# Optimization experiments

Measured on AMD Instinct MI355X. Metric: run time of the kernel, lower is better.

## Reference

```python
import jax, jax.numpy as jnp
import numpy as np
from jax import lax

H_IMG = 128; W_IMG = 128; C_IN = 200; NCLS = 16
N0 = H_IMG * W_IMG; N1 = 4096; N2 = 1024
K = 16  # neighbors(15) + 1 self loop, as in __init__
EPS = 1e-5
SLOPE = 0.01  # LeakyReLU default


def _leaky(x):
    return jnp.where(x >= 0, x, SLOPE * x)


def _bn1d(H, g, b):
    # BatchNorm1d in training mode: batch stats over node dim
    mu = H.mean(0)
    var = H.var(0)
    return (H - mu) * lax.rsqrt(var + EPS) * g + b


def _bn2d(x, g, b):
    mu = x.mean((0, 2, 3), keepdims=True)
    var = x.var((0, 2, 3), keepdims=True)
    return (x - mu) * lax.rsqrt(var + EPS) * g[None, :, None, None] + b[None, :, None, None]


def _ssconv(x, g, b, pw, pb, dw, db):
    # BN -> 1x1 pointwise conv -> LeakyReLU -> depthwise 5x5 conv -> LeakyReLU
    y = _bn2d(x, g, b)
    y = lax.conv_general_dilated(y, pw, (1, 1), 'SAME', dimension_numbers=('NCHW', 'OIHW', 'NCHW')) + pb[None, :, None, None]
    y = _leaky(y)
    c = dw.shape[0]
    y = lax.conv_general_dilated(y, dw, (1, 1), 'SAME', feature_group_count=c, dimension_numbers=('NCHW', 'OIHW', 'NCHW')) + db[None, :, None, None]
    return _leaky(y)


def _gcn(H, g, b, wt, bt, wo, bo, nbr):
    # GCNLayer_PyG, neighbors>0 branch. nbr: [N, K] neighbor indices (col), center broadcast (row)
    Hn = _bn1d(H, g, b)
    th = Hn @ wt + bt            # [N, 128]
    out = Hn @ wo + bo           # [N, F]
    A = jax.nn.sigmoid(jnp.einsum('nkd,nd->nk', th[nbr], th))  # sigmoid(<theta[col], theta[row]>)
    A = jax.nn.softmax(A, axis=1)                              # softmax over K neighbors
    agg = jnp.einsum('nk,nkf->nf', A, out[nbr])                # weighted neighbor aggregate
    return _leaky(agg), A


def _forward(x, hg, hb, hpw, hpb, hdw, hdb,
             e0_g, e0_b, e0_wt, e0_bt, e0_wo, e0_bo,
             e1_g, e1_b, e1_wt, e1_bt, e1_wo, e1_bo,
             d0_g, d0_b, d0_wt, d0_bt, d0_wo, d0_bo,
             tg, tb, tpw, tpb, tdw, tdb, ws, wb,
             S0, S1, Shat0, Shat1, nbr_a, nbr_b):
    x4 = x.transpose(2, 0, 1)[None]                 # [1, C, H, W]
    h0 = _ssconv(x4, hg, hb, hpw, hpb, hdw, hdb)    # [1, 128, H, W]
    H = h0[0].transpose(1, 2, 0).reshape(N0, -1)    # [N0, 128]
    enc0 = H
    H = Shat0 @ H                                   # pool to [N1, 128]
    H, A0 = _gcn(H, e0_g, e0_b, e0_wt, e0_bt, e0_wo, e0_bo, nbr_a)  # [N1, 64]
    enc1 = H
    H = Shat1 @ H                                   # pool to [N2, 64]
    H, A1 = _gcn(H, e1_g, e1_b, e1_wt, e1_bt, e1_wo, e1_bo, nbr_b)  # [N2, 32]
    # decoder
    H = S1 @ H                                      # unpool [N1, 32]
    H = jnp.concatenate([H, enc1], axis=-1)         # [N1, 96]
    H, Ad = _gcn(H, d0_g, d0_b, d0_wt, d0_bt, d0_wo, d0_bo, nbr_a)  # [N1, 64]
    H = S0 @ H                                      # unpool [N0, 64]
    H = jnp.concatenate([H, enc0], axis=-1)         # [N0, 192]
    t = H.reshape(1, H_IMG, W_IMG, -1).transpose(0, 3, 1, 2)
    f = _ssconv(t, tg, tb, tpw, tpb, tdw, tdb)      # [1, 128, H, W]
    f = f[0].transpose(1, 2, 0).reshape(N0, -1)
    Y = jax.nn.softmax(f @ ws + wb, axis=-1)        # [N0, NCLS]
    return Y


def setup_inputs() -> dict:
    key = jax.random.key(0)
    cnt = [0]
    def rn(shape, s=0.05):
        cnt[0] += 1
        return jax.random.normal(jax.random.fold_in(key, cnt[0]), shape, jnp.float32) * s
    x = rn((H_IMG, W_IMG, C_IN), 1.0)
    # balanced hierarchical assignment matrices (one-hot rows)
    S0 = jnp.zeros((N0, N1), jnp.float32).at[jnp.arange(N0), jnp.arange(N0) // (N0 // N1)].set(1.0)
    S1 = jnp.zeros((N1, N2), jnp.float32).at[jnp.arange(N1), jnp.arange(N1) // (N1 // N2)].set(1.0)
    Shat0 = (S0 / S0.sum(0, keepdims=True)).T
    Shat1 = (S1 / S1.sum(0, keepdims=True)).T
    # positions: pixel grid pooled through Shat (as in HiGCN.__init__)
    gx, gy = jnp.meshgrid(jnp.arange(H_IMG), jnp.arange(W_IMG), indexing='ij')
    pos = jnp.stack([gx, gy], -1).reshape(N0, 2).astype(jnp.float32)
    posA = Shat0 @ pos
    posB = Shat1 @ posA
    def knn(p):
        d = ((p[:, None, :] - p[None, :, :]) ** 2).sum(-1)
        return jnp.argsort(d, axis=1)[:, :K].astype(jnp.int32)  # self included (loop=True)
    nbr_a = knn(posA)  # [N1, K], used by enc0 and dec0
    nbr_b = knn(posB)  # [N2, K], used by enc1
    inp = dict(x=x, S0=S0, S1=S1, Shat0=Shat0, Shat1=Shat1, nbr_a=nbr_a, nbr_b=nbr_b)
    inp.update(hg=jnp.ones(C_IN), hb=jnp.zeros(C_IN), hpw=rn((128, C_IN, 1, 1)),
               hpb=jnp.zeros(128), hdw=rn((128, 1, 5, 5)), hdb=jnp.zeros(128))
    for tag, ci, co in (('e0', 128, 64), ('e1', 64, 32), ('d0', 96, 64)):
        inp[tag + '_g'] = jnp.ones(ci); inp[tag + '_b'] = jnp.zeros(ci)
        inp[tag + '_wt'] = rn((ci, 128)); inp[tag + '_bt'] = jnp.zeros(128)
        inp[tag + '_wo'] = rn((ci, co)); inp[tag + '_bo'] = jnp.zeros(co)
    inp.update(tg=jnp.ones(192), tb=jnp.zeros(192), tpw=rn((128, 192, 1, 1)),
               tpb=jnp.zeros(128), tdw=rn((128, 1, 5, 5)), tdb=jnp.zeros(128))
    inp.update(ws=rn((128, NCLS)), wb=jnp.zeros(NCLS))
    return inp


def reference(x, hg, hb, hpw, hpb, hdw, hdb,
              e0_g, e0_b, e0_wt, e0_bt, e0_wo, e0_bo,
              e1_g, e1_b, e1_wt, e1_bt, e1_wo, e1_bo,
              d0_g, d0_b, d0_wt, d0_bt, d0_wo, d0_bo,
              tg, tb, tpw, tpb, tdw, tdb, ws, wb,
              S0, S1, Shat0, Shat1, nbr_a, nbr_b):
    return _forward(x, hg, hb, hpw, hpb, hdw, hdb,
                    e0_g, e0_b, e0_wt, e0_bt, e0_wo, e0_bo,
                    e1_g, e1_b, e1_wt, e1_bt, e1_wo, e1_bo,
                    d0_g, d0_b, d0_wt, d0_bt, d0_wo, d0_bo,
                    tg, tb, tpw, tpb, tdw, tdb, ws, wb,
                    S0, S1, Shat0, Shat1, nbr_a, nbr_b)
```

## Files before the change

kernel.cpp:

```cpp
#include <hip/hip_runtime.h>
#include <hip/hip_bf16.h>
#include <math.h>

using bf16 = __hip_bfloat16;

#define H_IMG 128
#define W_IMG 128
#define C_IN  200
#define NCLS  16
#define N0    16384
#define N1    4096
#define N2    1024
#define KNB   16
#define EPS   1e-5f
#define SLOPE 0.01f

__device__ __forceinline__ float ldf(const float* p, long i) { return p[i]; }
__device__ __forceinline__ float ldf(const bf16* p, long i) { return __bfloat162float(p[i]); }
__device__ __forceinline__ float ldw(const void* p, long i, int fl) {
    return fl ? ((const float*)p)[i] : __bfloat162float(((const bf16*)p)[i]);
}
__device__ __forceinline__ float leaky(float v) { return v >= 0.f ? v : SLOPE * v; }

__device__ __forceinline__ float4 ld4(const float* p, long i) {
    return *reinterpret_cast<const float4*>(p + i);
}
__device__ __forceinline__ float4 ld4(const bf16* p, long i) {
    const ushort4 u = *reinterpret_cast<const ushort4*>(reinterpret_cast<const unsigned short*>(p) + i);
    float4 r;
    r.x = __uint_as_float((unsigned)u.x << 16);
    r.y = __uint_as_float((unsigned)u.y << 16);
    r.z = __uint_as_float((unsigned)u.z << 16);
    r.w = __uint_as_float((unsigned)u.w << 16);
    return r;
}

__device__ __forceinline__ int block_detect(const unsigned short* __restrict__ x) {
    __shared__ int cnt_s;
    if (threadIdx.x == 0) cnt_s = 0;
    __syncthreads();
    int cnt = 0;
    for (int i = threadIdx.x; i < 4096; i += blockDim.x) {
        unsigned short e = (unsigned short)((x[i] >> 7) & 0xFF);
        if (e >= 0xC0) cnt++;
    }
#pragma unroll
    for (int off = 32; off > 0; off >>= 1) cnt += __shfl_xor(cnt, off, 64);
    if ((threadIdx.x & 63) == 0) atomicAdd(&cnt_s, cnt);
    __syncthreads();
    return cnt_s > 32 ? 1 : 0;
}

__global__ __launch_bounds__(256) void bnx_kernel(const void* __restrict__ X, float2* __restrict__ part,
                                                  int* __restrict__ dflag) {
    int fl = block_detect((const unsigned short*)X);
    if (blockIdx.x == 0 && threadIdx.x == 0) *dflag = fl;
    int b = blockIdx.x, t = threadIdx.x;
    if (t >= C_IN) return;
    float s = 0.f, s2 = 0.f;
    if (fl) {
        const float* p = (const float*)X + (long)b * 64 * C_IN + t;
        for (int r = 0; r < 64; r++) { float v = p[(long)r * C_IN]; s += v; s2 += v * v; }
    } else {
        const bf16* p = (const bf16*)X + (long)b * 64 * C_IN + t;
        for (int r = 0; r < 64; r++) { float v = __bfloat162float(p[(long)r * C_IN]); s += v; s2 += v * v; }
    }
    part[(long)t * 256 + b] = make_float2(s, s2);
}

__device__ __forceinline__ void alphabeta_ld(const float2* __restrict__ partA, int npA, int splitC,
                                             const float2* __restrict__ partB, int npB,
                                             int Ci, float Pinv, const void* g, const void* b_,
                                             int fl, float* al, float* be) {
    int t = threadIdx.x;
    if (t < Ci) {
        const float2* src = (t < splitC) ? partA + (long)t * npA : partB + (long)(t - splitC) * npB;
        int np = (t < splitC) ? npA : npB;
        float s = 0.f, s2 = 0.f;
        const float4* p4 = (const float4*)src;
        for (int i = 0; i < (np >> 1); i++) { float4 v = p4[i]; s += v.x + v.z; s2 += v.y + v.w; }
        float mu = s * Pinv;
        float var = s2 * Pinv - mu * mu;
        float a = rsqrtf(var + EPS) * ldw(g, t, fl);
        al[t] = a;
        be[t] = ldw(b_, t, fl) - mu * a;
    }
    __syncthreads();
}

__device__ __forceinline__ void foldL(int j, const void* Wsrc, const void* bias,
                                      const float* al, const float* be,
                                      float* __restrict__ Wf, float* __restrict__ Bf,
                                      int Ci, int Co, int omajor, int fl, float* red) {
    int t = threadIdx.x;
    float acc = 0.f;
    for (int c = t; c < Ci; c += 256) {
        long idx = omajor ? (long)j * Ci + c : (long)c * Co + j;
        float w = ldw(Wsrc, idx, fl);
        Wf[(long)c * Co + j] = w * al[c];
        acc += w * be[c];
    }
    red[t] = acc; __syncthreads();
    for (int k = 128; k > 0; k >>= 1) { if (t < k) red[t] += red[t + k]; __syncthreads(); }
    if (t == 0) Bf[j] = ldw(bias, j, fl) + red[0];
}

__global__ __launch_bounds__(256) void bnfold_kernel(const float2* partA, int npA, int splitC,
                                                     const float2* partB, int npB, int P,
                                                     const void* g, const void* b_,
                                                     const void* Wt, const void* bias,
                                                     float* Wf, float* Bf, int Ci, int Co, int omajor,
                                                     const int* dflag) {
    __shared__ float al[256], be[256], red[256];
    int fl = *dflag;
    alphabeta_ld(partA, npA, splitC, partB, npB, Ci, 1.f / (float)P, g, b_, fl, al, be);
    foldL(blockIdx.x, Wt, bias, al, be, Wf, Bf, Ci, Co, omajor, fl, red);
}

__global__ __launch_bounds__(256) void bnfold2_kernel(const float2* partA, int npA, int splitC,
                                                      const float2* partB, int npB, int P,
                                                      const void* g, const void* b_,
                                                      const void* W1, const void* b1,
                                                      const void* W2, const void* b2,
                                                      float* Wf1, float* Bf1, float* Wf2, float* Bf2,
                                                      int Ci, int Co1, int Co2, const int* dflag) {
    __shared__ float al[256], be[256], red[256];
    int fl = *dflag;
    alphabeta_ld(partA, npA, splitC, partB, npB, Ci, 1.f / (float)P, g, b_, fl, al, be);
    int j = blockIdx.x;
    if (j < Co1) foldL(j, W1, b1, al, be, Wf1, Bf1, Ci, Co1, 0, fl, red);
    else         foldL(j - Co1, W2, b2, al, be, Wf2, Bf2, Ci, Co2, 0, fl, red);
}

template <typename T, int CI, int KT, int CAT>
__device__ __forceinline__ void gemmT_body(const T* __restrict__ In, const float* __restrict__ A2,
                                           const float* __restrict__ Wf, const float* __restrict__ Bf,
                                           float* __restrict__ Out) {
    __shared__ float wls[KT * 128];
    int t = threadIdx.x;
    int jq = t & 31, rp = t >> 5;
    int n0 = blockIdx.x * 16;
    int r0 = n0 + rp * 2, r1 = r0 + 1;
    float4 a0 = *reinterpret_cast<const float4*>(Bf + jq * 4);
    float4 a1 = a0;
    for (int kt = 0; kt < CI; kt += KT) {
        for (int e = t * 4; e < KT * 128; e += 1024)
            *reinterpret_cast<float4*>(&wls[e]) = *reinterpret_cast<const float4*>(&Wf[(long)kt * 128 + e]);
        __syncthreads();
        for (int cc = 0; cc < KT; cc += 4) {
            int c = kt + cc;
            float4 x0, x1;
            if (CAT) {
                if (c < 64) {
                    x0 = ld4(A2 + (long)(r0 >> 2) * 64, c);
                    x1 = ld4(A2 + (long)(r1 >> 2) * 64, c);
                } else {
                    x0 = ld4((const float*)In + (long)r0 * 128, c - 64);
                    x1 = ld4((const float*)In + (long)r1 * 128, c - 64);
                }
            } else {
                x0 = ld4(In + (long)r0 * CI, c);
                x1 = ld4(In + (long)r1 * CI, c);
            }
            const float* wp = &wls[cc * 128 + jq * 4];
            float4 w0 = *reinterpret_cast<const float4*>(wp);
            float4 w1 = *reinterpret_cast<const float4*>(wp + 128);
            float4 w2 = *reinterpret_cast<const float4*>(wp + 256);
            float4 w3 = *reinterpret_cast<const float4*>(wp + 384);
            a0.x += x0.x * w0.x; a0.y += x0.x * w0.y; a0.z += x0.x * w0.z; a0.w += x0.x * w0.w;
            a1.x += x1.x * w0.x; a1.y += x1.x * w0.y; a1.z += x1.x * w0.z; a1.w += x1.x * w0.w;
            a0.x += x0.y * w1.x; a0.y += x0.y * w1.y; a0.z += x0.y * w1.z; a0.w += x0.y * w1.w;
            a1.x += x1.y * w1.x; a1.y += x1.y * w1.y; a1.z += x1.y * w1.z; a1.w += x1.y * w1.w;
            a0.x += x0.z * w2.x; a0.y += x0.z * w2.y; a0.z += x0.z * w2.z; a0.w += x0.z * w2.w;
            a1.x += x1.z * w2.x; a1.y += x1.z * w2.y; a1.z += x1.z * w2.z; a1.w += x1.z * w2.w;
            a0.x += x0.w * w3.x; a0.y += x0.w * w3.y; a0.z += x0.w * w3.z; a0.w += x0.w * w3.w;
            a1.x += x1.w * w3.x; a1.y += x1.w * w3.y; a1.z += x1.w * w3.z; a1.w += x1.w * w3.w;
        }
        __syncthreads();
    }
    a0.x = leaky(a0.x); a0.y = leaky(a0.y); a0.z = leaky(a0.z); a0.w = leaky(a0.w);
    a1.x = leaky(a1.x); a1.y = leaky(a1.y); a1.z = leaky(a1.z); a1.w = leaky(a1.w);
    *reinterpret_cast<float4*>(Out + (long)r0 * 128 + jq * 4) = a0;
    *reinterpret_cast<float4*>(Out + (long)r1 * 128 + jq * 4) = a1;
}

__global__ __launch_bounds__(256) void gemmT_head_kernel(const void* In, const float* Wf, const float* Bf,
                                                         float* Out, const int* dflag) {
    if (*dflag) gemmT_body<float, C_IN, 40, 0>((const float*)In, nullptr, Wf, Bf, Out);
    else        gemmT_body<bf16,  C_IN, 40, 0>((const bf16*)In, nullptr, Wf, Bf, Out);
}

__global__ __launch_bounds__(256) void gemmT_tail_kernel(const float* InB, const float* InA,
                                                         const float* Wf, const float* Bf, float* Out) {
    gemmT_body<float, 192, 48, 1>(InB, InA, Wf, Bf, Out);
}

template <typename T, int ACT>
__device__ __forceinline__ void gemm4_body(const T* __restrict__ In, const float* __restrict__ Wf,
                                           const float* __restrict__ Bf, float* __restrict__ Out,
                                           int Ci, int Co, int blk) {
    int tid = blk * 256 + threadIdx.x;
    int Coq = Co >> 2;
    int n = tid / Coq;
    int j4 = (tid - n * Coq) << 2;
    const T* in = In + (long)n * Ci;
    const float* wp = Wf + j4;
    float4 acc = *reinterpret_cast<const float4*>(Bf + j4);
    for (int c = 0; c < Ci; c += 4) {
        float4 xv = ld4(in, c);
        float4 w0 = *reinterpret_cast<const float4*>(wp + (long)c * Co);
        float4 w1 = *reinterpret_cast<const float4*>(wp + (long)(c + 1) * Co);
        float4 w2 = *reinterpret_cast<const float4*>(wp + (long)(c + 2) * Co);
        float4 w3 = *reinterpret_cast<const float4*>(wp + (long)(c + 3) * Co);
        acc.x += xv.x * w0.x; acc.y += xv.x * w0.y; acc.z += xv.x * w0.z; acc.w += xv.x * w0.w;
        acc.x += xv.y * w1.x; acc.y += xv.y * w1.y; acc.z += xv.y * w1.z; acc.w += xv.y * w1.w;
        acc.x += xv.z * w2.x; acc.y += xv.z * w2.y; acc.z += xv.z * w2.z; acc.w += xv.z * w2.w;
        acc.x += xv.w * w3.x; acc.y += xv.w * w3.y; acc.z += xv.w * w3.z; acc.w += xv.w * w3.w;
    }
    if (ACT) { acc.x = leaky(acc.x); acc.y = leaky(acc.y); acc.z = leaky(acc.z); acc.w = leaky(acc.w); }
    *reinterpret_cast<float4*>(Out + (long)n * Co + j4) = acc;
}

template <int ACT, int SPLIT>
__device__ __forceinline__ void gemm4cat_body(const float* __restrict__ InA, int sA,
                                              const float* __restrict__ InB, int sB,
                                              const float* __restrict__ Wf, const float* __restrict__ Bf,
                                              float* __restrict__ Out, int Ci, int Co, int blk) {
    int tid = blk * 256 + threadIdx.x;
    int Coq = Co >> 2;
    int n = tid / Coq;
    int j4 = (tid - n * Coq) << 2;
    const float* ia = InA + (long)(n >> 2) * sA;
    const float* ib = InB + (long)n * sB;
    const float* wp = Wf + j4;
    float4 acc = *reinterpret_cast<const float4*>(Bf + j4);
    for (int c = 0; c < Ci; c += 4) {
        float4 xv = (c < SPLIT) ? *reinterpret_cast<const float4*>(ia + c)
                                : *reinterpret_cast<const float4*>(ib + (c - SPLIT));
        float4 w0 = *reinterpret_cast<const float4*>(wp + (long)c * Co);
        float4 w1 = *reinterpret_cast<const float4*>(wp + (long)(c + 1) * Co);
        float4 w2 = *reinterpret_cast<const float4*>(wp + (long)(c + 2) * Co);
        float4 w3 = *reinterpret_cast<const float4*>(wp + (long)(c + 3) * Co);
        acc.x += xv.x * w0.x; acc.y += xv.x * w0.y; acc.z += xv.x * w0.z; acc.w += xv.x * w0.w;
        acc.x += xv.y * w1.x; acc.y += xv.y * w1.y; acc.z += xv.y * w1.z; acc.w += xv.y * w1.w;
        acc.x += xv.z * w2.x; acc.y += xv.z * w2.y; acc.z += xv.z * w2.z; acc.w += xv.z * w2.w;
        acc.x += xv.w * w3.x; acc.y += xv.w * w3.y; acc.z += xv.w * w3.z; acc.w += xv.w * w3.w;
    }
    if (ACT) { acc.x = leaky(acc.x); acc.y = leaky(acc.y); acc.z = leaky(acc.z); acc.w = leaky(acc.w); }
    *reinterpret_cast<float4*>(Out + (long)n * Co + j4) = acc;
}

__global__ __launch_bounds__(256) void gemm2_f32_kernel(const float* In,
                                                        const float* W1, const float* B1, float* O1, int Co1,
                                                        const float* W2, const float* B2, float* O2, int Co2,
                                                        int Ci, int nb1) {
    int b = blockIdx.x;
    if (b < nb1) gemm4_body<float, 0>(In, W1, B1, O1, Ci, Co1, b);
    else         gemm4_body<float, 0>(In, W2, B2, O2, Ci, Co2, b - nb1);
}

template <int SPLIT>
__global__ __launch_bounds__(256) void gemm2cat_kernel(const float* InA, int sA, const float* InB, int sB,
                                                       const float* W1, const float* B1, float* O1, int Co1,
                                                       const float* W2, const float* B2, float* O2, int Co2,
                                                       int Ci, int nb1) {
    int b = blockIdx.x;
    if (b < nb1) gemm4cat_body<0, SPLIT>(InA, sA, InB, sB, W1, B1, O1, Ci, Co1, b);
    else         gemm4cat_body<0, SPLIT>(InA, sA, InB, sB, W2, B2, O2, Ci, Co2, b - nb1);
}

__device__ __forceinline__ void dw_load(const void* dwp, const void* dbp, float* wl, float* bl, int fl) {
    int t = threadIdx.x;
    for (int e = t; e < 25 * 128; e += 256) {
        int o = e / 25, i = e - o * 25;
        wl[i * 128 + o] = ldw(dwp, e, fl);
    }
    if (t < 128) bl[t] = ldw(dbp, t, fl);
}

__device__ __forceinline__ float4 dw_compute(int p, int o0, const float* __restrict__ In,
                                             const float* wl, const float* bl) {
    int h = p >> 7, w = p & 127;
    float4 acc = *reinterpret_cast<const float4*>(&bl[o0]);
#pragma unroll
    for (int dh = -2; dh <= 2; dh++) {
        int hh = h + dh;
        if ((unsigned)hh >= (unsigned)H_IMG) continue;
#pragma unroll
        for (int dv = -2; dv <= 2; dv++) {
            int ww = w + dv;
            if ((unsigned)ww >= (unsigned)W_IMG) continue;
            float4 iv = *reinterpret_cast<const float4*>(&In[(long)(((hh << 7) + ww) << 7) + o0]);
            float4 wv = *reinterpret_cast<const float4*>(&wl[((dh + 2) * 5 + (dv + 2)) * 128 + o0]);
            acc.x += iv.x * wv.x; acc.y += iv.y * wv.y; acc.z += iv.z * wv.z; acc.w += iv.w * wv.w;
        }
    }
    acc.x = leaky(acc.x); acc.y = leaky(acc.y); acc.z = leaky(acc.z); acc.w = leaky(acc.w);
    return acc;
}

__global__ __launch_bounds__(256) void dwpool_kernel(const float* __restrict__ In, const void* dwp, const void* dbp,
                                                     float* __restrict__ R1out, float* __restrict__ H1b,
                                                     float2* __restrict__ pE0, float2* __restrict__ pTb,
                                                     const int* dflag) {
    __shared__ float wl[25 * 128];
    __shared__ float bl[128];
    __shared__ float sm[8 * 132];
    int fl = *dflag;
    dw_load(dwp, dbp, wl, bl, fl);
    __syncthreads();
    int t = threadIdx.x;
    int o0 = (t & 31) << 2, pxl = t >> 5;
    float s = 0.f, s2 = 0.f, rs = 0.f, rs2 = 0.f;
    for (int it = 0; it < 4; it++) {
        int p = blockIdx.x * 32 + it * 8 + pxl;
        float4 acc = dw_compute(p, o0, In, wl, bl);
        *reinterpret_cast<float4*>(&R1out[(long)p * 128 + o0]) = acc;
        *reinterpret_cast<float4*>(&sm[pxl * 132 + o0]) = acc;
        __syncthreads();
        if (t < 128) {
#pragma unroll
            for (int g = 0; g < 2; g++) {
                float v0 = sm[(g * 4 + 0) * 132 + t], v1 = sm[(g * 4 + 1) * 132 + t];
                float v2 = sm[(g * 4 + 2) * 132 + t], v3 = sm[(g * 4 + 3) * 132 + t];
                float h = 0.25f * (v0 + v1 + v2 + v3);
                H1b[(long)(blockIdx.x * 8 + it * 2 + g) * 128 + t] = h;
                s += h; s2 += h * h;
                rs += v0 + v1 + v2 + v3;
                rs2 += v0 * v0 + v1 * v1 + v2 * v2 + v3 * v3;
            }
        }
        __syncthreads();
    }
    if (t < 128) {
        pE0[(long)t * 512 + blockIdx.x] = make_float2(s, s2);
        pTb[(long)t * 512 + blockIdx.x] = make_float2(rs, rs2);
    }
}

__global__ __launch_bounds__(256) void dwcls_kernel(const float* __restrict__ In, const void* dwp, const void* dbp,
                                                    const void* wsw, const void* wb, void* __restrict__ out,
                                                    const int* dflag) {
    __shared__ float wl[25 * 128];
    __shared__ float bl[128];
    __shared__ float cw[2048];
    __shared__ float F[8 * 132];
    int fl = *dflag;
    dw_load(dwp, dbp, wl, bl, fl);
    int t = threadIdx.x;
    for (int e = t; e < 2048; e += 256) cw[e] = ldw(wsw, e, fl);
    __syncthreads();
    int o0 = (t & 31) << 2, pxl = t >> 5;
    int p = blockIdx.x * 8 + pxl;
    float4 acc = dw_compute(p, o0, In, wl, bl);
    *reinterpret_cast<float4*>(&F[pxl * 132 + o0]) = acc;
    __syncthreads();
    if (t < 128) {
        int px = t >> 4, j = t & 15;
        float a = ldw(wb, j, fl);
        const float* fp = &F[px * 132];
#pragma unroll 8
        for (int c = 0; c < 128; c += 4) {
            float4 fv = *reinterpret_cast<const float4*>(fp + c);
            a += fv.x * cw[c * 16 + j] + fv.y * cw[(c + 1) * 16 + j]
               + fv.z * cw[(c + 2) * 16 + j] + fv.w * cw[(c + 3) * 16 + j];
        }
        float m = a;
#pragma unroll
        for (int s = 8; s > 0; s >>= 1) m = fmaxf(m, __shfl_xor(m, s, 16));
        float e = expf(a - m);
        float d = e;
#pragma unroll
        for (int s = 8; s > 0; s >>= 1) d += __shfl_xor(d, s, 16);
        float r = e / d;
        long oi = (long)(blockIdx.x * 8 + px) * 16 + j;
        if (fl) ((float*)out)[oi] = r;
        else ((bf16*)out)[oi] = __float2bfloat16(r);
    }
}

template <int MODE>
__global__ __launch_bounds__(256) void attn_fused_kernel(const float* __restrict__ th, const float* __restrict__ outm,
                                                         const int* __restrict__ nbr, float* __restrict__ dst, int co,
                                                         float* __restrict__ H2b,
                                                         float2* __restrict__ partP, float2* __restrict__ partS,
                                                         int snp) {
    int wid = threadIdx.x >> 6, l = threadIdx.x & 63;
    int n = blockIdx.x * 4 + wid;
    float r0 = th[(long)n * 128 + l];
    float r1 = th[(long)n * 128 + 64 + l];
    int mk[KNB];
    float av[KNB];
#pragma unroll
    for (int k = 0; k < KNB; k++) {
        int m = nbr[n * KNB + k];
        mk[k] = m;
        float v = r0 * th[(long)m * 128 + l] + r1 * th[(long)m * 128 + 64 + l];
#pragma unroll
        for (int off = 32; off > 0; off >>= 1) v += __shfl_xor(v, off, 64);
        av[k] = 1.f / (1.f + expf(-v));
    }
    float amax = av[0];
#pragma unroll
    for (int k = 1; k < KNB; k++) amax = fmaxf(amax, av[k]);
    float den = 0.f;
#pragma unroll
    for (int k = 0; k < KNB; k++) { av[k] = expf(av[k] - amax); den += av[k]; }
    float rden = 1.f / den;
    float val = 0.f;
    if (l < co) {
        float acc = 0.f;
#pragma unroll
        for (int k = 0; k < KNB; k++) acc += av[k] * outm[(long)mk[k] * co + l];
        val = leaky(acc * rden);
        dst[(long)n * co + l] = val;
    }
    __shared__ float sm[4][64];
    sm[wid][l] = (l < co) ? val : 0.f;
    __syncthreads();
    if (wid == 0 && l < co) {
        float a = sm[0][l], bb = sm[1][l], c = sm[2][l], d = sm[3][l];
        float su = a + bb + c + d;
        float sq = a * a + bb * bb + c * c + d * d;
        if (MODE == 0) {
            float h = 0.25f * su;
            H2b[(long)blockIdx.x * 64 + l] = h;
            partP[(long)l * snp + blockIdx.x] = make_float2(h, h * h);
            partS[(long)l * snp + blockIdx.x] = make_float2(su, sq);
        } else {
            partS[(long)l * snp + blockIdx.x] = make_float2(4.f * su, 4.f * sq);
        }
    }
}

extern "C" void kernel_launch(void* const* d_in, const int* in_sizes, int n_in,
                              void* d_out, int out_size, void* d_ws, size_t ws_size,
                              hipStream_t stream) {
    bool dict = (in_sizes[1] > 1000000);
    int I_x, I_nbr_a, I_nbr_b, I_hg, I_ws, I_e0, I_e1, I_d0, I_tg;
    if (dict) {
        I_x = 0; I_nbr_a = 5; I_nbr_b = 6; I_hg = 7; I_e0 = 13; I_e1 = 19; I_d0 = 25; I_tg = 31; I_ws = 37;
    } else {
        I_x = 0; I_hg = 1; I_e0 = 7; I_e1 = 13; I_d0 = 19; I_tg = 25; I_ws = 31; I_nbr_a = 37; I_nbr_b = 38;
    }
    const void* x    = d_in[I_x];
    const int* nbr_a = (const int*)d_in[I_nbr_a];
    const int* nbr_b = (const int*)d_in[I_nbr_b];
    const void* hg   = d_in[I_hg + 0];
    const void* hb   = d_in[I_hg + 1];
    const void* hpw  = d_in[I_hg + 2];
    const void* hpb  = d_in[I_hg + 3];
    const void* hdw  = d_in[I_hg + 4];
    const void* hdb  = d_in[I_hg + 5];
    const void* e0_g = d_in[I_e0 + 0];
    const void* e0_b = d_in[I_e0 + 1];
    const void* e0_wt= d_in[I_e0 + 2];
    const void* e0_bt= d_in[I_e0 + 3];
    const void* e0_wo= d_in[I_e0 + 4];
    const void* e0_bo= d_in[I_e0 + 5];
    const void* e1_g = d_in[I_e1 + 0];
    const void* e1_b = d_in[I_e1 + 1];
    const void* e1_wt= d_in[I_e1 + 2];
    const void* e1_bt= d_in[I_e1 + 3];
    const void* e1_wo= d_in[I_e1 + 4];
    const void* e1_bo= d_in[I_e1 + 5];
    const void* d0_g = d_in[I_d0 + 0];
    const void* d0_b = d_in[I_d0 + 1];
    const void* d0_wt= d_in[I_d0 + 2];
    const void* d0_bt= d_in[I_d0 + 3];
    const void* d0_wo= d_in[I_d0 + 4];
    const void* d0_bo= d_in[I_d0 + 5];
    const void* tg   = d_in[I_tg + 0];
    const void* tb   = d_in[I_tg + 1];
    const void* tpw  = d_in[I_tg + 2];
    const void* tpb  = d_in[I_tg + 3];
    const void* tdw  = d_in[I_tg + 4];
    const void* tdb  = d_in[I_tg + 5];
    const void* wsw  = d_in[I_ws + 0];
    const void* wb   = d_in[I_ws + 1];

    float* W = (float*)d_ws;
    float*  WF1    = W + 0;
    float*  BF1    = W + 25600;
    float*  WF2    = W + 25728;
    float*  BF2    = W + 33920;
    int*    dflag  = (int*)(W + 33984);
    float2* P_HEAD = (float2*)(W + 34048);
    float2* P_E0   = (float2*)(W + 136448);
    float2* P_Tb   = (float2*)(W + 267520);
    float2* P_E1   = (float2*)(W + 398592);
    float2* P_D0a  = (float2*)(W + 529664);
    float2* P_D0b  = (float2*)(W + 546048);
    float2* P_Ta   = (float2*)(W + 677120);
    float*  R0     = W + 808192;
    float*  R1     = R0 + (long)N0 * 128;
    float*  T1     = R1 + (long)N0 * 128;
    float*  H1b    = T1 + (long)N0 * 128;
    float*  THb    = H1b + (long)N1 * 128;
    float*  OUTb   = THb + (long)N1 * 128;
    float*  ENC1   = OUTb + (long)N1 * 64;
    float*  H2b    = ENC1 + (long)N1 * 64;
    float*  HDb    = H2b + (long)N2 * 64;
    float*  HDEC   = HDb + (long)N2 * 32;

    bnx_kernel<<<256, 256, 0, stream>>>(x, P_HEAD, dflag);
    bnfold_kernel<<<128, 256, 0, stream>>>(P_HEAD, 256, C_IN, P_HEAD, 256, N0,
                                           hg, hb, hpw, hpb, WF1, BF1, C_IN, 128, 1, dflag);
    gemmT_head_kernel<<<1024, 256, 0, stream>>>(x, WF1, BF1, R0, dflag);
    dwpool_kernel<<<512, 256, 0, stream>>>(R0, hdw, hdb, R1, H1b, P_E0, P_Tb, dflag);
    bnfold2_kernel<<<192, 256, 0, stream>>>(P_E0, 512, 128, P_E0, 512, N1, e0_g, e0_b,
                                            e0_wt, e0_bt, e0_wo, e0_bo,
                                            WF1, BF1, WF2, BF2, 128, 128, 64, dflag);
    gemm2_f32_kernel<<<768, 256, 0, stream>>>(H1b, WF1, BF1, THb, 128, WF2, BF2, OUTb, 64, 128, 512);
    attn_fused_kernel<0><<<1024, 256, 0, stream>>>(THb, OUTb, nbr_a, ENC1, 64, H2b, P_E1, P_D0b, 1024);
    bnfold2_kernel<<<160, 256, 0, stream>>>(P_E1, 1024, 64, P_E1, 1024, N2, e1_g, e1_b,
                                            e1_wt, e1_bt, e1_wo, e1_bo,
                                            WF1, BF1, WF2, BF2, 64, 128, 32, dflag);
    gemm2_f32_kernel<<<160, 256, 0, stream>>>(H2b, WF1, BF1, THb, 128, WF2, BF2, OUTb, 32, 64, 128);
    attn_fused_kernel<1><<<256, 256, 0, stream>>>(THb, OUTb, nbr_b, HDb, 32, nullptr, nullptr, P_D0a, 256);
    bnfold2_kernel<<<192, 256, 0, stream>>>(P_D0a, 256, 32, P_D0b, 1024, N1, d0_g, d0_b,
                                            d0_wt, d0_bt, d0_wo, d0_bo,
                                            WF1, BF1, WF2, BF2, 96, 128, 64, dflag);
    gemm2cat_kernel<32><<<768, 256, 0, stream>>>(HDb, 32, ENC1, 64,
                                                 WF1, BF1, THb, 128, WF2, BF2, OUTb, 64, 96, 512);
    attn_fused_kernel<2><<<1024, 256, 0, stream>>>(THb, OUTb, nbr_a, HDEC, 64, nullptr, nullptr, P_Ta, 1024);
    bnfold_kernel<<<128, 256, 0, stream>>>(P_Ta, 1024, 64, P_Tb, 512, N0,
                                           tg, tb, tpw, tpb, WF1, BF1, 192, 128, 1, dflag);
    gemmT_tail_kernel<<<1024, 256, 0, stream>>>(R1, HDEC, WF1, BF1, T1);
    dwcls_kernel<<<2048, 256, 0, stream>>>(T1, tdw, tdb, wsw, wb, d_out, dflag);
}
```

Baseline: 949.2 us.

## Fuse BN-fold weight scaling into GEMM kernels and drop separate bnfold launches

Removes the bnfold/bnfold2 kernels. Each GEMM block now recomputes the BN statistics, the folded bias and the scaled weights on the fly while staging weights into LDS. A prep kernel pre-transposes the head and tail pointwise weights once. The separate gemm2 kernels are replaced by one LDS-tiled GEMM template that computes two rows per thread. This cuts four kernel launches and their global round-trips, at the cost of every block redundantly reducing the partial statistics and computing the bias dot product.

```diff
diff --git a/kernel.cpp b/kernel.cpp
--- a/kernel.cpp
+++ b/kernel.cpp
@@ -15,13 +15,10 @@
 #define EPS   1e-5f
 #define SLOPE 0.01f
 
-__device__ __forceinline__ float ldf(const float* p, long i) { return p[i]; }
-__device__ __forceinline__ float ldf(const bf16* p, long i) { return __bfloat162float(p[i]); }
+__device__ __forceinline__ float leaky(float v) { return v >= 0.f ? v : SLOPE * v; }
 __device__ __forceinline__ float ldw(const void* p, long i, int fl) {
     return fl ? ((const float*)p)[i] : __bfloat162float(((const bf16*)p)[i]);
 }
-__device__ __forceinline__ float leaky(float v) { return v >= 0.f ? v : SLOPE * v; }
-
 __device__ __forceinline__ float4 ld4(const float* p, long i) {
     return *reinterpret_cast<const float4*>(p + i);
 }
@@ -34,6 +31,9 @@
     r.w = __uint_as_float((unsigned)u.w << 16);
     return r;
 }
+__device__ __forceinline__ float4 ld4w(const void* p, long i, int fl) {
+    return fl ? ld4((const float*)p, i) : ld4((const bf16*)p, i);
+}
 
 __device__ __forceinline__ int block_detect(const unsigned short* __restrict__ x) {
     __shared__ int cnt_s;
@@ -51,10 +51,27 @@
     return cnt_s > 32 ? 1 : 0;
 }
 
-__global__ __launch_bounds__(256) void bnx_kernel(const void* __restrict__ X, float2* __restrict__ part,
-                                                  int* __restrict__ dflag) {
+__global__ __launch_bounds__(256) void prep_kernel(const void* __restrict__ x,
+                                                   const void* __restrict__ hpw, const void* __restrict__ tpw,
+                                                   float* __restrict__ WHc, float* __restrict__ WTc,
+                                                   int* __restrict__ dflag) {
+    int fl = block_detect((const unsigned short*)x);
+    if (blockIdx.x == 0 && threadIdx.x == 0) *dflag = fl;
+    if (blockIdx.x < 8) {
+        for (long e = blockIdx.x * 256 + threadIdx.x; e < 128L * C_IN; e += 8 * 256) {
+            int j = (int)(e / C_IN), c = (int)(e - (long)j * C_IN);
+            WHc[(long)c * 128 + j] = ldw(hpw, e, fl);
+        }
+    } else {
+        for (long e = (blockIdx.x - 8) * 256 + threadIdx.x; e < 128L * 192; e += 8 * 256) {
+            int j = (int)(e / 192), c = (int)(e - (long)j * 192);
+            WTc[(long)c * 128 + j] = ldw(tpw, e, fl);
+        }
+    }
+}
+
+__global__ __launch_bounds__(256) void bnx_kernel(const void* __restrict__ X, float2* __restrict__ part) {
     int fl = block_detect((const unsigned short*)X);
-    if (blockIdx.x == 0 && threadIdx.x == 0) *dflag = fl;
     int b = blockIdx.x, t = threadIdx.x;
     if (t >= C_IN) return;
     float s = 0.f, s2 = 0.f;
@@ -68,105 +85,78 @@
     part[(long)t * 256 + b] = make_float2(s, s2);
 }
 
-__device__ __forceinline__ void alphabeta_ld(const float2* __restrict__ partA, int npA, int splitC,
-                                             const float2* __restrict__ partB, int npB,
-                                             int Ci, float Pinv, const void* g, const void* b_,
-                                             int fl, float* al, float* be) {
+template <typename TIN, int CI, int CO, int KT, int ACT, int CAT, int SPLIT, int WRAW>
+__device__ __forceinline__ void gemmF_body(const TIN* __restrict__ In, int sIn,
+                                           const float* __restrict__ A2, int sA2,
+                                           const void* __restrict__ Wsrc, const void* __restrict__ bvec,
+                                           const float2* __restrict__ pA, int npA, int splitC,
+                                           const float2* __restrict__ pB, int npB, float Pinv,
+                                           const void* __restrict__ g, const void* __restrict__ bt,
+                                           int fl, float* __restrict__ Out, int blk, float* smem) {
+    float* al = smem;
+    float* be = smem + 256;
+    float* bs = smem + 512;
+    float* wls = smem + 640;
     int t = threadIdx.x;
-    if (t < Ci) {
-        const float2* src = (t < splitC) ? partA + (long)t * npA : partB + (long)(t - splitC) * npB;
+    if (t < CI) {
+        const float2* src = (t < splitC) ? pA + (long)t * npA : pB + (long)(t - splitC) * npB;
         int np = (t < splitC) ? npA : npB;
         float s = 0.f, s2 = 0.f;
         const float4* p4 = (const float4*)src;
         for (int i = 0; i < (np >> 1); i++) { float4 v = p4[i]; s += v.x + v.z; s2 += v.y + v.w; }
         float mu = s * Pinv;
         float var = s2 * Pinv - mu * mu;
-        float a = rsqrtf(var + EPS) * ldw(g, t, fl);
-        al[t] = a;
-        be[t] = ldw(b_, t, fl) - mu * a;
-    }
-    __syncthreads();
-}
-
-__device__ __forceinline__ void foldL(int j, const void* Wsrc, const void* bias,
-                                      const float* al, const float* be,
-                                      float* __restrict__ Wf, float* __restrict__ Bf,
-                                      int Ci, int Co, int omajor, int fl, float* red) {
-    int t = threadIdx.x;
-    float acc = 0.f;
-    for (int c = t; c < Ci; c += 256) {
-        long idx = omajor ? (long)j * Ci + c : (long)c * Co + j;
-        float w = ldw(Wsrc, idx, fl);
-        Wf[(long)c * Co + j] = w * al[c];
-        acc += w * be[c];
-    }
-    red[t] = acc; __syncthreads();
-    for (int k = 128; k > 0; k >>= 1) { if (t < k) red[t] += red[t + k]; __syncthreads(); }
-    if (t == 0) Bf[j] = ldw(bias, j, fl) + red[0];
-}
-
-__global__ __launch_bounds__(256) void bnfold_kernel(const float2* partA, int npA, int splitC,
-                                                     const float2* partB, int npB, int P,
-                                                     const void* g, const void* b_,
-                                                     const void* Wt, const void* bias,
-                                                     float* Wf, float* Bf, int Ci, int Co, int omajor,
-                                                     const int* dflag) {
-    __shared__ float al[256], be[256], red[256];
-    int fl = *dflag;
-    alphabeta_ld(partA, npA, splitC, partB, npB, Ci, 1.f / (float)P, g, b_, fl, al, be);
-    foldL(blockIdx.x, Wt, bias, al, be, Wf, Bf, Ci, Co, omajor, fl, red);
-}
-
-__global__ __launch_bounds__(256) void bnfold2_kernel(const float2* partA, int npA, int splitC,
-                                                      const float2* partB, int npB, int P,
-                                                      const void* g, const void* b_,
-                                                      const void* W1, const void* b1,
-                                                      const void* W2, const void* b2,
-                                                      float* Wf1, float* Bf1, float* Wf2, float* Bf2,
-                                                      int Ci, int Co1, int Co2, const int* dflag) {
-    __shared__ float al[256], be[256], red[256];
-    int fl = *dflag;
-    alphabeta_ld(partA, npA, splitC, partB, npB, Ci, 1.f / (float)P, g, b_, fl, al, be);
-    int j = blockIdx.x;
-    if (j < Co1) foldL(j, W1, b1, al, be, Wf1, Bf1, Ci, Co1, 0, fl, red);
-    else         foldL(j - Co1, W2, b2, al, be, Wf2, Bf2, Ci, Co2, 0, fl, red);
-}
-
-template <typename T, int CI, int KT, int CAT>
-__device__ __forceinline__ void gemmT_body(const T* __restrict__ In, const float* __restrict__ A2,
-                                           const float* __restrict__ Wf, const float* __restrict__ Bf,
-                                           float* __restrict__ Out) {
-    __shared__ float wls[KT * 128];
-    int t = threadIdx.x;
-    int jq = t & 31, rp = t >> 5;
-    int n0 = blockIdx.x * 16;
-    int r0 = n0 + rp * 2, r1 = r0 + 1;
-    float4 a0 = *reinterpret_cast<const float4*>(Bf + jq * 4);
+        float aa = rsqrtf(var + EPS) * ldw(g, t, fl);
+        al[t] = aa;
+        be[t] = ldw(bt, t, fl) - mu * aa;
+    }
+    __syncthreads();
+    if (t < CO) {
+        float s = ldw(bvec, t, fl);
+        for (int c = 0; c < CI; c++) {
+            float w = WRAW ? ldw(Wsrc, (long)c * CO + t, fl) : ((const float*)Wsrc)[(long)c * CO + t];
+            s += w * be[c];
+        }
+        bs[t] = s;
+    }
+    __syncthreads();
+    constexpr int NQ = CO / 4;
+    constexpr int SH = (NQ == 32) ? 5 : (NQ == 16) ? 4 : 3;
+    constexpr int L2CO = (CO == 128) ? 7 : (CO == 64) ? 6 : 5;
+    constexpr int RPB = 512 / NQ;
+    int jq = t & (NQ - 1), rp = t >> SH;
+    int r0 = blk * RPB + rp * 2, r1 = r0 + 1;
+    float4 a0 = *reinterpret_cast<float4*>(&bs[jq * 4]);
     float4 a1 = a0;
     for (int kt = 0; kt < CI; kt += KT) {
-        for (int e = t * 4; e < KT * 128; e += 1024)
-            *reinterpret_cast<float4*>(&wls[e]) = *reinterpret_cast<const float4*>(&Wf[(long)kt * 128 + e]);
+        for (int e4 = t * 4; e4 < KT * CO; e4 += 1024) {
+            int cc = e4 >> L2CO, j4 = e4 & (CO - 1);
+            float aa = al[kt + cc];
+            float4 w = WRAW ? ld4w(Wsrc, (long)(kt + cc) * CO + j4, fl)
+                            : ld4((const float*)Wsrc, (long)(kt + cc) * CO + j4);
+            *reinterpret_cast<float4*>(&wls[e4]) = make_float4(w.x * aa, w.y * aa, w.z * aa, w.w * aa);
+        }
         __syncthreads();
         for (int cc = 0; cc < KT; cc += 4) {
             int c = kt + cc;
             float4 x0, x1;
             if (CAT) {
-                if (c < 64) {
-                    x0 = ld4(A2 + (long)(r0 >> 2) * 64, c);
-                    x1 = ld4(A2 + (long)(r1 >> 2) * 64, c);
+                if (c < SPLIT) {
+                    x0 = ld4(A2 + (long)(r0 >> 2) * sA2, c);
+                    x1 = ld4(A2 + (long)(r1 >> 2) * sA2, c);
                 } else {
-                    x0 = ld4((const float*)In + (long)r0 * 128, c - 64);
-                    x1 = ld4((const float*)In + (long)r1 * 128, c - 64);
+                    x0 = ld4((const float*)(const void*)In + (long)r0 * sIn, c - SPLIT);
+                    x1 = ld4((const float*)(const void*)In + (long)r1 * sIn, c - SPLIT);
                 }
             } else {
-                x0 = ld4(In + (long)r0 * CI, c);
-                x1 = ld4(In + (long)r1 * CI, c);
+                x0 = ld4(In + (long)r0 * sIn, c);
+                x1 = ld4(In + (long)r1 * sIn, c);
             }
-            const float* wp = &wls[cc * 128 + jq * 4];
-            float4 w0 = *reinterpret_cast<const float4*>(wp);
-            float4 w1 = *reinterpret_cast<const float4*>(wp + 128);
-            float4 w2 = *reinterpret_cast<const float4*>(wp + 256);
-            float4 w3 = *reinterpret_cast<const float4*>(wp + 384);
+            const float* wp = &wls[cc * CO + jq * 4];
+            float4 w0 = *(const float4*)wp;
+            float4 w1 = *(const float4*)(wp + CO);
+            float4 w2 = *(const float4*)(wp + 2 * CO);
+            float4 w3 = *(const float4*)(wp + 3 * CO);
             a0.x += x0.x * w0.x; a0.y += x0.x * w0.y; a0.z += x0.x * w0.z; a0.w += x0.x * w0.w;
             a1.x += x1.x * w0.x; a1.y += x1.x * w0.y; a1.z += x1.x * w0.z; a1.w += x1.x * w0.w;
             a0.x += x0.y * w1.x; a0.y += x0.y * w1.y; a0.z += x0.y * w1.z; a0.w += x0.y * w1.w;
@@ -178,95 +168,86 @@
         }
         __syncthreads();
     }
-    a0.x = leaky(a0.x); a0.y = leaky(a0.y); a0.z = leaky(a0.z); a0.w = leaky(a0.w);
-    a1.x = leaky(a1.x); a1.y = leaky(a1.y); a1.z = leaky(a1.z); a1.w = leaky(a1.w);
-    *reinterpret_cast<float4*>(Out + (long)r0 * 128 + jq * 4) = a0;
-    *reinterpret_cast<float4*>(Out + (long)r1 * 128 + jq * 4) = a1;
-}
-
-__global__ __launch_bounds__(256) void gemmT_head_kernel(const void* In, const float* Wf, const float* Bf,
-                                                         float* Out, const int* dflag) {
-    if (*dflag) gemmT_body<float, C_IN, 40, 0>((const float*)In, nullptr, Wf, Bf, Out);
-    else        gemmT_body<bf16,  C_IN, 40, 0>((const bf16*)In, nullptr, Wf, Bf, Out);
-}
-
-__global__ __launch_bounds__(256) void gemmT_tail_kernel(const float* InB, const float* InA,
-                                                         const float* Wf, const float* Bf, float* Out) {
-    gemmT_body<float, 192, 48, 1>(InB, InA, Wf, Bf, Out);
-}
-
-template <typename T, int ACT>
-__device__ __forceinline__ void gemm4_body(const T* __restrict__ In, const float* __restrict__ Wf,
-                                           const float* __restrict__ Bf, float* __restrict__ Out,
-                                           int Ci, int Co, int blk) {
-    int tid = blk * 256 + threadIdx.x;
-    int Coq = Co >> 2;
-    int n = tid / Coq;
-    int j4 = (tid - n * Coq) << 2;
-    const T* in = In + (long)n * Ci;
-    const float* wp = Wf + j4;
-    float4 acc = *reinterpret_cast<const float4*>(Bf + j4);
-    for (int c = 0; c < Ci; c += 4) {
-        float4 xv = ld4(in, c);
-        float4 w0 = *reinterpret_cast<const float4*>(wp + (long)c * Co);
-        float4 w1 = *reinterpret_cast<const float4*>(wp + (long)(c + 1) * Co);
-        float4 w2 = *reinterpret_cast<const float4*>(wp + (long)(c + 2) * Co);
-        float4 w3 = *reinterpret_cast<const float4*>(wp + (long)(c + 3) * Co);
-        acc.x += xv.x * w0.x; acc.y += xv.x * w0.y; acc.z += xv.x * w0.z; acc.w += xv.x * w0.w;
-        acc.x += xv.y * w1.x; acc.y += xv.y * w1.y; acc.z += xv.y * w1.z; acc.w += xv.y * w1.w;
-        acc.x += xv.z * w2.x; acc.y += xv.z * w2.y; acc.z += xv.z * w2.z; acc.w += xv.z * w2.w;
-        acc.x += xv.w * w3.x; acc.y += xv.w * w3.y; acc.z += xv.w * w3.z; acc.w += xv.w * w3.w;
-    }
-    if (ACT) { acc.x = leaky(acc.x); acc.y = leaky(acc.y); acc.z = leaky(acc.z); acc.w = leaky(acc.w); }
-    *reinterpret_cast<float4*>(Out + (long)n * Co + j4) = acc;
-}
-
-template <int ACT, int SPLIT>
-__device__ __forceinline__ void gemm4cat_body(const float* __restrict__ InA, int sA,
-                                              const float* __restrict__ InB, int sB,
-                                              const float* __restrict__ Wf, const float* __restrict__ Bf,
-                                              float* __restrict__ Out, int Ci, int Co, int blk) {
-    int tid = blk * 256 + threadIdx.x;
-    int Coq = Co >> 2;
-    int n = tid / Coq;
-    int j4 = (tid - n * Coq) << 2;
-    const float* ia = InA + (long)(n >> 2) * sA;
-    const float* ib = InB + (long)n * sB;
-    const float* wp = Wf + j4;
-    float4 acc = *reinterpret_cast<const float4*>(Bf + j4);
-    for (int c = 0; c < Ci; c += 4) {
-        float4 xv = (c < SPLIT) ? *reinterpret_cast<const float4*>(ia + c)
-                                : *reinterpret_cast<const float4*>(ib + (c - SPLIT));
-        float4 w0 = *reinterpret_cast<const float4*>(wp + (long)c * Co);
-        float4 w1 = *reinterpret_cast<const float4*>(wp + (long)(c + 1) * Co);
-        float4 w2 = *reinterpret_cast<const float4*>(wp + (long)(c + 2) * Co);
-        float4 w3 = *reinterpret_cast<const float4*>(wp + (long)(c + 3) * Co);
-        acc.x += xv.x * w0.x; acc.y += xv.x * w0.y; acc.z += xv.x * w0.z; acc.w += xv.x * w0.w;
-        acc.x += xv.y * w1.x; acc.y += xv.y * w1.y; acc.z += xv.y * w1.z; acc.w += xv.y * w1.w;
-        acc.x += xv.z * w2.x; acc.y += xv.z * w2.y; acc.z += xv.z * w2.z; acc.w += xv.z * w2.w;
-        acc.x += xv.w * w3.x; acc.y += xv.w * w3.y; acc.z += xv.w * w3.z; acc.w += xv.w * w3.w;
-    }
-    if (ACT) { acc.x = leaky(acc.x); acc.y = leaky(acc.y); acc.z = leaky(acc.z); acc.w = leaky(acc.w); }
-    *reinterpret_cast<float4*>(Out + (long)n * Co + j4) = acc;
-}
-
-__global__ __launch_bounds__(256) void gemm2_f32_kernel(const float* In,
-                                                        const float* W1, const float* B1, float* O1, int Co1,
-                                                        const float* W2, const float* B2, float* O2, int Co2,
-                                                        int Ci, int nb1) {
-    int b = blockIdx.x;
-    if (b < nb1) gemm4_body<float, 0>(In, W1, B1, O1, Ci, Co1, b);
-    else         gemm4_body<float, 0>(In, W2, B2, O2, Ci, Co2, b - nb1);
-}
-
-template <int SPLIT>
-__global__ __launch_bounds__(256) void gemm2cat_kernel(const float* InA, int sA, const float* InB, int sB,
-                                                       const float* W1, const float* B1, float* O1, int Co1,
-                                                       const float* W2, const float* B2, float* O2, int Co2,
-                                                       int Ci, int nb1) {
-    int b = blockIdx.x;
-    if (b < nb1) gemm4cat_body<0, SPLIT>(InA, sA, InB, sB, W1, B1, O1, Ci, Co1, b);
-    else         gemm4cat_body<0, SPLIT>(InA, sA, InB, sB, W2, B2, O2, Ci, Co2, b - nb1);
+    if (ACT) {
+        a0.x = leaky(a0.x); a0.y = leaky(a0.y); a0.z = leaky(a0.z); a0.w = leaky(a0.w);
+        a1.x = leaky(a1.x); a1.y = leaky(a1.y); a1.z = leaky(a1.z); a1.w = leaky(a1.w);
+    }
+    *reinterpret_cast<float4*>(Out + (long)r0 * CO + jq * 4) = a0;
+    *reinterpret_cast<float4*>(Out + (long)r1 * CO + jq * 4) = a1;
+}
+
+__global__ __launch_bounds__(256) void gemmF_head_kernel(const void* x, const float* WHc, const void* hpb,
+                                                         const float2* pH, const void* hg, const void* hb_,
+                                                         float* R0, const int* dflag) {
+    extern __shared__ float smem[];
+    int fl = *dflag;
+    if (fl) gemmF_body<float, C_IN, 128, 40, 1, 0, 0, 0>((const float*)x, C_IN, nullptr, 0, WHc, hpb,
+                                                         pH, 256, C_IN, pH, 256, 1.f / (float)N0,
+                                                         hg, hb_, 1, R0, (int)blockIdx.x, smem);
+    else    gemmF_body<bf16, C_IN, 128, 40, 1, 0, 0, 0>((const bf16*)x, C_IN, nullptr, 0, WHc, hpb,
+                                                        pH, 256, C_IN, pH, 256, 1.f / (float)N0,
+                                                        hg, hb_, 0, R0, (int)blockIdx.x, smem);
+}
+
+__global__ __launch_bounds__(256) void gemmF_e0_kernel(const float* H1b,
+                                                       const void* wt, const void* bt_, const void* wo, const void* bo,
+                                                       const float2* pE0, const void* g, const void* b_,
+                                                       float* TH, float* OU, const int* dflag) {
+    extern __shared__ float smem[];
+    int fl = *dflag;
+    if (blockIdx.x < 256)
+        gemmF_body<float, 128, 128, 64, 0, 0, 0, 1>(H1b, 128, nullptr, 0, wt, bt_,
+                                                    pE0, 512, 128, pE0, 512, 1.f / (float)N1,
+                                                    g, b_, fl, TH, (int)blockIdx.x, smem);
+    else
+        gemmF_body<float, 128, 64, 128, 0, 0, 0, 1>(H1b, 128, nullptr, 0, wo, bo,
+                                                    pE0, 512, 128, pE0, 512, 1.f / (float)N1,
+                                                    g, b_, fl, OU, (int)blockIdx.x - 256, smem);
+}
+
+__global__ __launch_bounds__(256) void gemmF_e1_kernel(const float* H2b,
+                                                       const void* wt, const void* bt_, const void* wo, const void* bo,
+                                                       const float2* pE1, const void* g, const void* b_,
+                                                       float* TH, float* OU, const int* dflag) {
+    extern __shared__ float smem[];
+    int fl = *dflag;
+    if (blockIdx.x < 64)
+        gemmF_body<float, 64, 128, 64, 0, 0, 0, 1>(H2b, 64, nullptr, 0, wt, bt_,
+                                                   pE1, 1024, 64, pE1, 1024, 1.f / (float)N2,
+                                                   g, b_, fl, TH, (int)blockIdx.x, smem);
+    else
+        gemmF_body<float, 64, 32, 64, 0, 0, 0, 1>(H2b, 64, nullptr, 0, wo, bo,
+                                                  pE1, 1024, 64, pE1, 1024, 1.f / (float)N2,
+                                                  g, b_, fl, OU, (int)blockIdx.x - 64, smem);
+}
+
+__global__ __launch_bounds__(256) void gemmF_d0_kernel(const float* ENC1, const float* HDb,
+                                                       const void* wt, const void* bt_, const void* wo, const void* bo,
+                                                       const float2* pD0a, const float2* pD0b,
+                                                       const void* g, const void* b_,
+                                                       float* TH, float* OU, const int* dflag) {
+    extern __shared__ float smem[];
+    int fl = *dflag;
+    if (blockIdx.x < 256)
+        gemmF_body<float, 96, 128, 48, 0, 1, 32, 1>(ENC1, 64, HDb, 32, wt, bt_,
+                                                    pD0a, 256, 32, pD0b, 1024, 1.f / (float)N1,
+                                                    g, b_, fl, TH, (int)blockIdx.x, smem);
+    else
+        gemmF_body<float, 96, 64, 96, 0, 1, 32, 1>(ENC1, 64, HDb, 32, wo, bo,
+                                                   pD0a, 256, 32, pD0b, 1024, 1.f / (float)N1,
+                                                   g, b_, fl, OU, (int)blockIdx.x - 256, smem);
+}
+
+__global__ __launch_bounds__(256) void gemmF_tail_kernel(const float* R1, const float* HDEC,
+                                                         const float* WTc, const void* tpb,
+                                                         const float2* pTa, const float2* pTb,
+                                                         const void* g, const void* b_,
+                                                         float* T1, const int* dflag) {
+    extern __shared__ float smem[];
+    int fl = *dflag;
+    gemmF_body<float, 192, 128, 48, 1, 1, 64, 0>(R1, 128, HDEC, 64, WTc, tpb,
+                                                 pTa, 1024, 64, pTb, 512, 1.f / (float)N0,
+                                                 g, b_, fl, T1, (int)blockIdx.x, smem);
 }
 
 __device__ __forceinline__ void dw_load(const void* dwp, const void* dbp, float* wl, float* bl, int fl) {
@@ -480,19 +461,17 @@
     const void* wb   = d_in[I_ws + 1];
 
     float* W = (float*)d_ws;
-    float*  WF1    = W + 0;
-    float*  BF1    = W + 25600;
-    float*  WF2    = W + 25728;
-    float*  BF2    = W + 33920;
-    int*    dflag  = (int*)(W + 33984);
-    float2* P_HEAD = (float2*)(W + 34048);
-    float2* P_E0   = (float2*)(W + 136448);
-    float2* P_Tb   = (float2*)(W + 267520);
-    float2* P_E1   = (float2*)(W + 398592);
-    float2* P_D0a  = (float2*)(W + 529664);
-    float2* P_D0b  = (float2*)(W + 546048);
-    float2* P_Ta   = (float2*)(W + 677120);
-    float*  R0     = W + 808192;
+    float*  WHc    = W + 0;
+    float*  WTc    = W + 25600;
+    int*    dflag  = (int*)(W + 50176);
+    float2* P_HEAD = (float2*)(W + 50240);
+    float2* P_E0   = (float2*)(W + 152640);
+    float2* P_Tb   = (float2*)(W + 283712);
+    float2* P_E1   = (float2*)(W + 414784);
+    float2* P_D0a  = (float2*)(W + 545856);
+    float2* P_D0b  = (float2*)(W + 562240);
+    float2* P_Ta   = (float2*)(W + 693312);
+    float*  R0     = W + 824384;
     float*  R1     = R0 + (long)N0 * 128;
     float*  T1     = R1 + (long)N0 * 128;
     float*  H1b    = T1 + (long)N0 * 128;
@@ -503,29 +482,25 @@
     float*  HDb    = H2b + (long)N2 * 64;
     float*  HDEC   = HDb + (long)N2 * 32;
 
-    bnx_kernel<<<256, 256, 0, stream>>>(x, P_HEAD, dflag);
-    bnfold_kernel<<<128, 256, 0, stream>>>(P_HEAD, 256, C_IN, P_HEAD, 256, N0,
-                                           hg, hb, hpw, hpb, WF1, BF1, C_IN, 128, 1, dflag);
-    gemmT_head_kernel<<<1024, 256, 0, stream>>>(x, WF1, BF1, R0, dflag);
+    const int SM_HEAD = (640 + 40 * 128) * 4;
+    const int SM_E0   = (640 + 8192) * 4;
+    const int SM_E1   = (640 + 8192) * 4;
+    const int SM_D0   = (640 + 6144) * 4;
+    const int SM_TAIL = (640 + 6144) * 4;
+
+    prep_kernel<<<16, 256, 0, stream>>>(x, hpw, tpw, WHc, WTc, dflag);
+    bnx_kernel<<<256, 256, 0, stream>>>(x, P_HEAD);
+    gemmF_head_kernel<<<1024, 256, SM_HEAD, stream>>>(x, WHc, hpb, P_HEAD, hg, hb, R0, dflag);
     dwpool_kernel<<<512, 256, 0, stream>>>(R0, hdw, hdb, R1, H1b, P_E0, P_Tb, dflag);
-    bnfold2_kernel<<<192, 256, 0, stream>>>(P_E0, 512, 128, P_E0, 512, N1, e0_g, e0_b,
-                                            e0_wt, e0_bt, e0_wo, e0_bo,
-                                            WF1, BF1, WF2, BF2, 128, 128, 64, dflag);
-    gemm2_f32_kernel<<<768, 256, 0, stream>>>(H1b, WF1, BF1, THb, 128, WF2, BF2, OUTb, 64, 128, 512);
+    gemmF_e0_kernel<<<384, 256, SM_E0, stream>>>(H1b, e0_wt, e0_bt, e0_wo, e0_bo,
+                                                 P_E0, e0_g, e0_b, THb, OUTb, dflag);
     attn_fused_kernel<0><<<1024, 256, 0, stream>>>(THb, OUTb, nbr_a, ENC1, 64, H2b, P_E1, P_D0b, 1024);
-    bnfold2_kernel<<<160, 256, 0, stream>>>(P_E1, 1024, 64, P_E1, 1024, N2, e1_g, e1_b,
-                                            e1_wt, e1_bt, e1_wo, e1_bo,
-                                            WF1, BF1, WF2, BF2, 64, 128, 32, dflag);
-    gemm2_f32_kernel<<<160, 256, 0, stream>>>(H2b, WF1, BF1, THb, 128, WF2, BF2, OUTb, 32, 64, 128);
+    gemmF_e1_kernel<<<80, 256, SM_E1, stream>>>(H2b, e1_wt, e1_bt, e1_wo, e1_bo,
+                                                P_E1, e1_g, e1_b, THb, OUTb, dflag);
     attn_fused_kernel<1><<<256, 256, 0, stream>>>(THb, OUTb, nbr_b, HDb, 32, nullptr, nullptr, P_D0a, 256);
-    bnfold2_kernel<<<192, 256, 0, stream>>>(P_D0a, 256, 32, P_D0b, 1024, N1, d0_g, d0_b,
-                                            d0_wt, d0_bt, d0_wo, d0_bo,
-                                            WF1, BF1, WF2, BF2, 96, 128, 64, dflag);
-    gemm2cat_kernel<32><<<768, 256, 0, stream>>>(HDb, 32, ENC1, 64,
-                                                 WF1, BF1, THb, 128, WF2, BF2, OUTb, 64, 96, 512);
+    gemmF_d0_kernel<<<384, 256, SM_D0, stream>>>(ENC1, HDb, d0_wt, d0_bt, d0_wo, d0_bo,
+                                                 P_D0a, P_D0b, d0_g, d0_b, THb, OUTb, dflag);
     attn_fused_kernel<2><<<1024, 256, 0, stream>>>(THb, OUTb, nbr_a, HDEC, 64, nullptr, nullptr, P_Ta, 1024);
-    bnfold_kernel<<<128, 256, 0, stream>>>(P_Ta, 1024, 64, P_Tb, 512, N0,
-                                           tg, tb, tpw, tpb, WF1, BF1, 192, 128, 1, dflag);
-    gemmT_tail_kernel<<<1024, 256, 0, stream>>>(R1, HDEC, WF1, BF1, T1);
+    gemmF_tail_kernel<<<1024, 256, SM_TAIL, stream>>>(R1, HDEC, WTc, tpb, P_Ta, P_Tb, tg, tb, T1, dflag);
     dwcls_kernel<<<2048, 256, 0, stream>>>(T1, tdw, tdb, wsw, wb, d_out, dflag);
 }
```

After: 1.168 ms. +23.0%, slower.
